# Kernel optimization log

Measured on AMD Instinct MI355X. Metric: run time of the kernel, lower is better.

Reference implementation:

```python
import jax, jax.numpy as jnp
import numpy as np


def setup_inputs() -> dict:
    key = jax.random.key(0)
    k1, k2 = jax.random.split(key)
    embed1 = jax.random.normal(k1, (4096, 32), dtype=jnp.float32)
    embed2 = jax.random.normal(k2, (4096, 32), dtype=jnp.float32)
    return {"embed1": embed1, "embed2": embed2}


def reference(embed1, embed2):
    # Chebyshev (L-inf) pairwise distance matrix: [N, M]
    # diff: [N, M, D] broadcasted subtract, abs, max over feature dim D
    return jnp.max(jnp.abs(embed1[:, None, :] - embed2[None, :, :]), axis=2)
```

## Files before the change

### kernel.cpp

```cpp
#include <hip/hip_runtime.h>

#define FD 32
#define TILE 64
#define LSTRIDE (TILE + 4)

__global__ __launch_bounds__(256) void cheb_kernel(
    const float* __restrict__ A, const float* __restrict__ B,
    float* __restrict__ C, int N, int M)
{
    __shared__ float sA[FD][LSTRIDE];
    __shared__ float sB[FD][LSTRIDE];

    const int tid = threadIdx.x;
    const int r0 = blockIdx.y * TILE;
    const int c0 = blockIdx.x * TILE;

#pragma unroll
    for (int k = 0; k < 2; ++k) {
        const int idx = tid + k * 256;
        const int row = idx >> 3;
        const int dq  = (idx & 7) * 4;
        const float4 va = *reinterpret_cast<const float4*>(A + (size_t)(r0 + row) * FD + dq);
        sA[dq + 0][row] = va.x;
        sA[dq + 1][row] = va.y;
        sA[dq + 2][row] = va.z;
        sA[dq + 3][row] = va.w;
        const float4 vb = *reinterpret_cast<const float4*>(B + (size_t)(c0 + row) * FD + dq);
        sB[dq + 0][row] = vb.x;
        sB[dq + 1][row] = vb.y;
        sB[dq + 2][row] = vb.z;
        sB[dq + 3][row] = vb.w;
    }
    __syncthreads();

    const int tx = tid & 15;
    const int ty = tid >> 4;

    float acc[4][4];
#pragma unroll
    for (int i = 0; i < 4; ++i)
#pragma unroll
        for (int j = 0; j < 4; ++j)
            acc[i][j] = 0.0f;

#pragma unroll
    for (int d = 0; d < FD; ++d) {
        const float4 a4 = *reinterpret_cast<const float4*>(&sA[d][ty * 4]);
        const float4 b4 = *reinterpret_cast<const float4*>(&sB[d][tx * 4]);
        const float a[4] = {a4.x, a4.y, a4.z, a4.w};
        const float b[4] = {b4.x, b4.y, b4.z, b4.w};
#pragma unroll
        for (int i = 0; i < 4; ++i)
#pragma unroll
            for (int j = 0; j < 4; ++j)
                acc[i][j] = fmaxf(acc[i][j], fabsf(a[i] - b[j]));
    }

#pragma unroll
    for (int i = 0; i < 4; ++i) {
        const int row = r0 + ty * 4 + i;
        float4 o;
        o.x = acc[i][0]; o.y = acc[i][1]; o.z = acc[i][2]; o.w = acc[i][3];
        *reinterpret_cast<float4*>(C + (size_t)row * M + c0 + tx * 4) = o;
    }
}

extern "C" void kernel_launch(void* const* d_in, const int* in_sizes, int n_in,
                              void* d_out, int out_size, void* d_ws, size_t ws_size,
                              hipStream_t stream) {
    const float* A = (const float*)d_in[0];
    const float* B = (const float*)d_in[1];
    float* C = (float*)d_out;
    const int N = in_sizes[0] / FD;
    const int M = in_sizes[1] / FD;
    dim3 grid(M / TILE, N / TILE);
    cheb_kernel<<<grid, 256, 0, stream>>>(A, B, C, N, M);
}
```

Baseline: 25.15 us.

## Replace LDS-tiled kernel with register-resident B columns and packed-math inner loop

Drops the shared-memory tiling. Each thread now keeps two negated B rows in registers and streams A rows directly from global memory, which become wave-uniform broadcast loads. The inner loop uses inline-asm v_pk_add_f32 together with v_max3_f32 using abs modifiers, cutting the VALU instruction count per element pair. This removes LDS traffic and barriers, but uses more registers and relies on scalar or broadcast global loads of A being cheap.

```diff
diff --git a/kernel.cpp b/kernel.cpp
--- a/kernel.cpp
+++ b/kernel.cpp
@@ -1,67 +1,59 @@
 #include <hip/hip_runtime.h>
 
 #define FD 32
-#define TILE 64
-#define LSTRIDE (TILE + 4)
+#define RPB 32
+#define CPT 2
+#define BLK 256
+
+__device__ __forceinline__ float2 pk_add(float2 a, float2 b) {
+    float2 r;
+    asm("v_pk_add_f32 %0, %1, %2" : "=v"(r) : "v"(a), "v"(b));
+    return r;
+}
+__device__ __forceinline__ float max3abs(float a, float x, float y) {
+    float r;
+    asm("v_max3_f32 %0, %1, abs(%2), abs(%3)" : "=v"(r) : "v"(a), "v"(x), "v"(y));
+    return r;
+}
 
 __global__ __launch_bounds__(256) void cheb_kernel(
     const float* __restrict__ A, const float* __restrict__ B,
-    float* __restrict__ C, int N, int M)
+    float* __restrict__ C, int M)
 {
-    __shared__ float sA[FD][LSTRIDE];
-    __shared__ float sB[FD][LSTRIDE];
+    const int tid = threadIdx.x;
+    const int c  = blockIdx.x * (BLK * CPT) + tid * CPT;
+    const int r0 = blockIdx.y * RPB;
 
-    const int tid = threadIdx.x;
-    const int r0 = blockIdx.y * TILE;
-    const int c0 = blockIdx.x * TILE;
-
+    float2 nb0[16], nb1[16];
+    {
+        const float* b0 = B + (size_t)c * FD;
 #pragma unroll
-    for (int k = 0; k < 2; ++k) {
-        const int idx = tid + k * 256;
-        const int row = idx >> 3;
-        const int dq  = (idx & 7) * 4;
-        const float4 va = *reinterpret_cast<const float4*>(A + (size_t)(r0 + row) * FD + dq);
-        sA[dq + 0][row] = va.x;
-        sA[dq + 1][row] = va.y;
-        sA[dq + 2][row] = va.z;
-        sA[dq + 3][row] = va.w;
-        const float4 vb = *reinterpret_cast<const float4*>(B + (size_t)(c0 + row) * FD + dq);
-        sB[dq + 0][row] = vb.x;
-        sB[dq + 1][row] = vb.y;
-        sB[dq + 2][row] = vb.z;
-        sB[dq + 3][row] = vb.w;
-    }
-    __syncthreads();
-
-    const int tx = tid & 15;
-    const int ty = tid >> 4;
-
-    float acc[4][4];
-#pragma unroll
-    for (int i = 0; i < 4; ++i)
-#pragma unroll
-        for (int j = 0; j < 4; ++j)
-            acc[i][j] = 0.0f;
-
-#pragma unroll
-    for (int d = 0; d < FD; ++d) {
-        const float4 a4 = *reinterpret_cast<const float4*>(&sA[d][ty * 4]);
-        const float4 b4 = *reinterpret_cast<const float4*>(&sB[d][tx * 4]);
-        const float a[4] = {a4.x, a4.y, a4.z, a4.w};
-        const float b[4] = {b4.x, b4.y, b4.z, b4.w};
-#pragma unroll
-        for (int i = 0; i < 4; ++i)
-#pragma unroll
-            for (int j = 0; j < 4; ++j)
-                acc[i][j] = fmaxf(acc[i][j], fabsf(a[i] - b[j]));
+        for (int q = 0; q < 8; ++q) {
+            const float4 v = *reinterpret_cast<const float4*>(b0 + q * 4);
+            nb0[2 * q + 0] = make_float2(-v.x, -v.y);
+            nb0[2 * q + 1] = make_float2(-v.z, -v.w);
+            const float4 w = *reinterpret_cast<const float4*>(b0 + FD + q * 4);
+            nb1[2 * q + 0] = make_float2(-w.x, -w.y);
+            nb1[2 * q + 1] = make_float2(-w.z, -w.w);
+        }
     }
 
+#pragma unroll 2
+    for (int r = 0; r < RPB; ++r) {
+        const float* arow = A + (size_t)(r0 + r) * FD;
+        float acc0 = 0.0f, acc1 = 0.0f;
 #pragma unroll
-    for (int i = 0; i < 4; ++i) {
-        const int row = r0 + ty * 4 + i;
-        float4 o;
-        o.x = acc[i][0]; o.y = acc[i][1]; o.z = acc[i][2]; o.w = acc[i][3];
-        *reinterpret_cast<float4*>(C + (size_t)row * M + c0 + tx * 4) = o;
+        for (int q = 0; q < 8; ++q) {
+            const float4 av = *reinterpret_cast<const float4*>(arow + q * 4);
+            const float2 a01 = make_float2(av.x, av.y);
+            const float2 a23 = make_float2(av.z, av.w);
+            float2 d;
+            d = pk_add(a01, nb0[2 * q + 0]); acc0 = max3abs(acc0, d.x, d.y);
+            d = pk_add(a23, nb0[2 * q + 1]); acc0 = max3abs(acc0, d.x, d.y);
+            d = pk_add(a01, nb1[2 * q + 0]); acc1 = max3abs(acc1, d.x, d.y);
+            d = pk_add(a23, nb1[2 * q + 1]); acc1 = max3abs(acc1, d.x, d.y);
+        }
+        *reinterpret_cast<float2*>(C + (size_t)(r0 + r) * M + c) = make_float2(acc0, acc1);
     }
 }
 
@@ -73,6 +65,6 @@
     float* C = (float*)d_out;
     const int N = in_sizes[0] / FD;
     const int M = in_sizes[1] / FD;
-    dim3 grid(M / TILE, N / TILE);
-    cheb_kernel<<<grid, 256, 0, stream>>>(A, B, C, N, M);
+    dim3 grid(M / (BLK * CPT), N / RPB);
+    cheb_kernel<<<grid, BLK, 0, stream>>>(A, B, C, M);
 }
```

New measurement: 52.02 us. +106.9%, slower.
